# Kernel tuning notes

Hardware: AMD Instinct MI355X
Metric: run time of the kernel (lower is better)

The kernel has to match this reference:

```python
import jax, jax.numpy as jnp
import numpy as np

N, E = 50000, 600000
IN_DIM, H, D = 256, 4, 128
NEG_SLOPE = 0.2


def setup_inputs() -> dict:
    key = jax.random.key(0)
    ks = jax.random.split(key, 9)
    x = jax.random.normal(ks[0], (N, IN_DIM), dtype=jnp.float32)
    src = jax.random.randint(ks[1], (E,), 0, N, dtype=jnp.int32)
    dst = jax.random.randint(ks[2], (E,), 0, N, dtype=jnp.int32)
    # layer 0: in=256 -> H*D=512; layer 1: in=H*D=512 -> H*D=512
    s0 = 1.0 / np.sqrt(IN_DIM)
    s1 = 1.0 / np.sqrt(H * D)
    W0 = jax.random.normal(ks[3], (IN_DIM, H * D), dtype=jnp.float32) * s0
    al0 = jax.random.normal(ks[4], (H, D), dtype=jnp.float32) * s1
    ar0 = jax.random.normal(ks[5], (H, D), dtype=jnp.float32) * s1
    W1 = jax.random.normal(ks[6], (H * D, H * D), dtype=jnp.float32) * s1
    al1 = jax.random.normal(ks[7], (H, D), dtype=jnp.float32) * s1
    ar1 = jax.random.normal(ks[8], (H, D), dtype=jnp.float32) * s1
    return {"x": x, "src": src, "dst": dst,
            "W0": W0, "al0": al0, "ar0": ar0,
            "W1": W1, "al1": al1, "ar1": ar1}


def gat_conv(x, W, al, ar, src, dst):
    """One DGL-style GATConv layer. x:[N,in] -> out:[N,H,D] (post relu)."""
    h = (x @ W).reshape(N, H, D)                       # fc, no bias
    el = jnp.sum(h * al, axis=-1)                      # [N,H]
    er = jnp.sum(h * ar, axis=-1)                      # [N,H]
    e = jax.nn.leaky_relu(el[src] + er[dst], NEG_SLOPE)  # [E,H]
    # edge softmax over incoming edges of each dst node (numerically stable)
    m = jax.ops.segment_max(e, dst, num_segments=N)    # [N,H]
    m = jnp.where(jnp.isfinite(m), m, 0.0)             # empty segments -> -inf
    ex = jnp.exp(e - m[dst])                           # [E,H]
    denom = jax.ops.segment_sum(ex, dst, num_segments=N)  # [N,H]
    alpha = ex / denom[dst]                            # [E,H]
    msg = alpha[:, :, None] * h[src]                   # [E,H,D]
    rst = jax.ops.segment_sum(msg, dst, num_segments=N)  # [N,H,D]
    return jax.nn.relu(rst)                            # activation=F.relu


def reference(x, src, dst, W0, al0, ar0, W1, al1, ar1):
    h = gat_conv(x, W0, al0, ar0, src, dst)            # [N,H,D]
    h = h.reshape(N, H * D)                            # flatten(1)
    h = gat_conv(h, W1, al1, ar1, src, dst)            # [N,H,D]
    return h.mean(axis=1)                              # mean over heads -> [N,D]
```

## Files before the change

kernel.cpp:

```cpp
#include <hip/hip_runtime.h>

#define NN 50000
#define NE 600000
#define DD 128
#define HD 512
#define NB 196

typedef unsigned short u16;
typedef __attribute__((ext_vector_type(8))) short short8;
typedef __attribute__((ext_vector_type(4))) float floatx4;

__device__ inline float b2f(u16 u) {
  return __uint_as_float(((unsigned int)u) << 16);
}
__device__ inline u16 f2b(float f) {
  unsigned int u = __float_as_uint(f);
  u = u + 0x7FFFu + ((u >> 16) & 1u);
  return (u16)(u >> 16);
}

__device__ inline void load_lds16(const u16* g, u16* l) {
  __builtin_amdgcn_global_load_lds(
      (const __attribute__((address_space(1))) unsigned int*)(uintptr_t)g,
      (__attribute__((address_space(3))) unsigned int*)(uintptr_t)l,
      16, 0, 0);
}

__global__ void zero_k(int* __restrict__ p, int n) {
  int i = blockIdx.x * 256 + threadIdx.x;
  if (i < n) p[i] = 0;
}

__global__ void transpose_k(const float* __restrict__ W, u16* __restrict__ Wt, int K) {
  int idx = blockIdx.x * 256 + threadIdx.x;
  if (idx >= K * 512) return;
  int k = idx >> 9, n = idx & 511;
  Wt[n * K + k] = f2b(W[idx]);
}

__global__ void count_k(const int* __restrict__ dst, int* __restrict__ counts) {
  int e = blockIdx.x * 256 + threadIdx.x;
  if (e < NE) atomicAdd(&counts[dst[e]], 1);
}

__global__ __launch_bounds__(256) void blockscan_k(const int* __restrict__ counts,
                                                   int* __restrict__ rowp,
                                                   int* __restrict__ bsums) {
  __shared__ int tmp[256];
  int t = threadIdx.x;
  int i = blockIdx.x * 256 + t;
  int v = (i < NN) ? counts[i] : 0;
  tmp[t] = v;
  __syncthreads();
  for (int off = 1; off < 256; off <<= 1) {
    int u = (t >= off) ? tmp[t - off] : 0;
    __syncthreads();
    tmp[t] += u;
    __syncthreads();
  }
  if (i < NN) rowp[i] = tmp[t] - v;
  if (t == 255) bsums[blockIdx.x] = tmp[t];
}

__global__ __launch_bounds__(256) void bscan_k(const int* __restrict__ bsums,
                                               int* __restrict__ boffs) {
  __shared__ int tmp[256];
  int t = threadIdx.x;
  int v = (t < NB) ? bsums[t] : 0;
  tmp[t] = v;
  __syncthreads();
  for (int off = 1; off < 256; off <<= 1) {
    int u = (t >= off) ? tmp[t - off] : 0;
    __syncthreads();
    tmp[t] += u;
    __syncthreads();
  }
  if (t < NB) boffs[t] = tmp[t] - v;
}

__global__ void addoff_k(int* __restrict__ rowp, int* __restrict__ cursor,
                         const int* __restrict__ boffs) {
  int i = blockIdx.x * 256 + threadIdx.x;
  if (i < NN) {
    int v = rowp[i] + boffs[blockIdx.x];
    rowp[i] = v;
    cursor[i] = v;
  }
  if (i == 0) rowp[NN] = NE;
}

__global__ void scatter_k(const int* __restrict__ src, const int* __restrict__ dst,
                          int* __restrict__ cursor, int* __restrict__ csrs) {
  int e = blockIdx.x * 256 + threadIdx.x;
  if (e < NE) {
    int d = dst[e];
    int pos = atomicAdd(&cursor[d], 1);
    csrs[pos] = src[e];
  }
}

template <int K, bool A_F32>
__global__ __launch_bounds__(512) void gemm_el_er(
    const void* __restrict__ Ap, const u16* __restrict__ Wt,
    const float* __restrict__ al, const float* __restrict__ ar,
    u16* __restrict__ h, float* __restrict__ el, float* __restrict__ er) {
  __shared__ u16 Wt_s[2][512 * 32];

  const int tid = threadIdx.x;
  const int w = tid >> 6, lane = tid & 63, quad = lane >> 4, l16 = lane & 15;
  const int rg = w >> 1, cg = w & 1;
  const int bm = blockIdx.x;

  floatx4 acc[16] = {};

  const int rowA = bm * 64 + rg * 16 + l16;
  const long arow = (rowA < NN) ? rowA : (NN - 1);

  const int drow = lane >> 2;
  const int q8 = ((lane & 3) ^ ((lane >> 3) & 3)) * 8;
  const int p4 = (quad ^ ((l16 >> 1) & 3)) * 8;

  const float* Af = (const float*)Ap;
  const u16* Ab = (const u16*)Ap;

#define ISSUE_DMA(kk, sel)                                                  \
  {                                                                         \
    _Pragma("unroll") for (int rr = 0; rr < 4; ++rr) {                      \
      const int rbase = rr * 128 + w * 16;                                  \
      load_lds16(Wt + (long)(rbase + drow) * K + (kk) + q8,                 \
                 &Wt_s[sel][rbase * 32]);                                   \
    }                                                                       \
  }

  floatx4 a0A, a1A, a0B, a1B;
  short8 rawA, rawB;

#define ISSUE_A(kk, a0r, a1r, rawr)                                         \
  {                                                                         \
    if (A_F32) {                                                            \
      a0r = *(const floatx4*)(Af + arow * K + (kk) + quad * 8);             \
      a1r = *(const floatx4*)(Af + arow * K + (kk) + quad * 8 + 4);         \
    } else {                                                                \
      rawr = *(const short8*)(Ab + arow * K + (kk) + quad * 8);             \
    }                                                                       \
  }

#define CVT_A(af, a0r, a1r, rawr)                                           \
  short8 af;                                                                \
  {                                                                         \
    if (A_F32) {                                                            \
      u16 tmp[8];                                                           \
      _Pragma("unroll") for (int j = 0; j < 4; ++j) tmp[j] = f2b(a0r[j]);   \
      _Pragma("unroll") for (int j = 0; j < 4; ++j) tmp[4 + j] = f2b(a1r[j]); \
      af = *(short8*)tmp;                                                   \
    } else {                                                                \
      af = rawr;                                                            \
    }                                                                       \
  }

#define WAIT_PREV()                                                         \
  {                                                                         \
    if (A_F32)                                                              \
      asm volatile("s_waitcnt vmcnt(6)" ::: "memory");                      \
    else                                                                    \
      asm volatile("s_waitcnt vmcnt(5)" ::: "memory");                      \
  }

  const int T = K / 32;

  ISSUE_A(0, a0A, a1A, rawA);
  ISSUE_DMA(0, 0);

  for (int t = 0; t < T; t += 2) {
    {
      const int k1 = (t + 1) * 32;
      ISSUE_A(k1, a0B, a1B, rawB);
      ISSUE_DMA(k1, 1);
      WAIT_PREV();
      __builtin_amdgcn_s_barrier();
      CVT_A(af, a0A, a1A, rawA);
#pragma unroll
      for (int ct = 0; ct < 16; ++ct) {
        short8 bf = *(const short8*)(&Wt_s[0][(cg * 256 + ct * 16 + l16) * 32 + p4]);
        acc[ct] = __builtin_amdgcn_mfma_f32_16x16x32_bf16(af, bf, acc[ct], 0, 0, 0);
      }
      __builtin_amdgcn_sched_barrier(0);
      __builtin_amdgcn_s_barrier();
    }
    {
      const int t2 = (t + 2 < T) ? t + 2 : T - 1;
      const int k2 = t2 * 32;
      ISSUE_A(k2, a0A, a1A, rawA);
      ISSUE_DMA(k2, 0);
      WAIT_PREV();
      __builtin_amdgcn_s_barrier();
      CVT_A(af, a0B, a1B, rawB);
#pragma unroll
      for (int ct = 0; ct < 16; ++ct) {
        short8 bf = *(const short8*)(&Wt_s[1][(cg * 256 + ct * 16 + l16) * 32 + p4]);
        acc[ct] = __builtin_amdgcn_mfma_f32_16x16x32_bf16(af, bf, acc[ct], 0, 0, 0);
      }
      __builtin_amdgcn_sched_barrier(0);
      __builtin_amdgcn_s_barrier();
    }
  }

#undef ISSUE_DMA
#undef ISSUE_A
#undef CVT_A
#undef WAIT_PREV

  float alv[16], arv[16];
#pragma unroll
  for (int ct = 0; ct < 16; ++ct) {
    int col = cg * 256 + ct * 16 + l16;
    alv[ct] = al[col];
    arv[ct] = ar[col];
  }
#pragma unroll
  for (int reg = 0; reg < 4; ++reg) {
    const int r = bm * 64 + rg * 16 + quad * 4 + reg;
    float pel[2] = {0.f, 0.f}, per_[2] = {0.f, 0.f};
#pragma unroll
    for (int ct = 0; ct < 16; ++ct) {
      int hh = ct >> 3;
      float v = acc[ct][reg];
      pel[hh] += v * alv[ct];
      per_[hh] += v * arv[ct];
    }
#pragma unroll
    for (int m = 1; m < 16; m <<= 1) {
      pel[0] += __shfl_xor(pel[0], m, 64);
      pel[1] += __shfl_xor(pel[1], m, 64);
      per_[0] += __shfl_xor(per_[0], m, 64);
      per_[1] += __shfl_xor(per_[1], m, 64);
    }
    if (r < NN) {
#pragma unroll
      for (int ct = 0; ct < 16; ++ct)
        h[(long)r * HD + cg * 256 + ct * 16 + l16] = f2b(acc[ct][reg]);
      if (l16 == 0) {
        el[r * 4 + cg * 2] = pel[0];
        el[r * 4 + cg * 2 + 1] = pel[1];
        er[r * 4 + cg * 2] = per_[0];
        er[r * 4 + cg * 2 + 1] = per_[1];
      }
    }
  }
}

template <int MODE>
__global__ __launch_bounds__(256) void aggregate(
    const u16* __restrict__ h, const float* __restrict__ el,
    const float* __restrict__ er, const int* __restrict__ rowp,
    const int* __restrict__ csrs, u16* __restrict__ ob, float* __restrict__ of) {
  __shared__ float w_s[4][64][4];
  const int wv = threadIdx.x >> 6, lane = threadIdx.x & 63;
  const int n = blockIdx.x * 4 + wv;
  if (n >= NN) return;
  const int base = rowp[n];
  const int deg = rowp[n + 1] - base;
  const int head = lane >> 4;

  if (deg == 0) {
    if (MODE == 0) {
      short8 z = {};
      *(short8*)(ob + (long)n * HD + lane * 8) = z;
    } else if (lane < 16) {
      floatx4 z = {};
      __builtin_nontemporal_store(z, (floatx4*)(of + (long)n * DD + lane * 8));
      __builtin_nontemporal_store(z, (floatx4*)(of + (long)n * DD + lane * 8 + 4));
    }
    return;
  }

  const floatx4 er4 = *(const floatx4*)(er + n * 4);

  float acc[8] = {0.f, 0.f, 0.f, 0.f, 0.f, 0.f, 0.f, 0.f};
  float sm0 = 0.f, sm1 = 0.f, sm2 = 0.f, sm3 = 0.f;

  for (int c0 = 0; c0 < deg; c0 += 64) {
    const int cnt = min(deg - c0, 64);

    const int l = c0 + lane;
    const int idx = csrs[base + ((l < deg) ? l : (deg - 1))];
    const floatx4 el4 = *(const floatx4*)(el + (long)idx * 4);
    floatx4 w4;
#pragma unroll
    for (int j = 0; j < 4; ++j) {
      float e = el4[j] + er4[j];
      e = (e > 0.f) ? e : 0.2f * e;
      w4[j] = (l < deg) ? __expf(e) : 0.f;
    }
    sm0 += w4[0];
    sm1 += w4[1];
    sm2 += w4[2];
    sm3 += w4[3];
    *(floatx4*)(&w_s[wv][lane][0]) = w4;

    for (int i = 0; i < cnt; i += 8) {
      short8 hv[8];
#pragma unroll
      for (int u = 0; u < 8; ++u) {
        const int s = __builtin_amdgcn_readlane(idx, i + u);
        hv[u] = *(const short8*)(h + (long)s * HD + lane * 8);
      }
#pragma unroll
      for (int u = 0; u < 8; ++u) {
        const float w = w_s[wv][i + u][head];
#pragma unroll
        for (int j = 0; j < 8; ++j) acc[j] += w * b2f((u16)hv[u][j]);
      }
    }
  }

#pragma unroll
  for (int m = 1; m < 64; m <<= 1) {
    sm0 += __shfl_xor(sm0, m, 64);
    sm1 += __shfl_xor(sm1, m, 64);
    sm2 += __shfl_xor(sm2, m, 64);
    sm3 += __shfl_xor(sm3, m, 64);
  }
  const float sm = (head == 0) ? sm0 : (head == 1) ? sm1 : (head == 2) ? sm2 : sm3;

  const float inv = 1.f / sm;
#pragma unroll
  for (int j = 0; j < 8; ++j) acc[j] = fmaxf(acc[j] * inv, 0.f);

  if (MODE == 0) {
    u16 ub[8];
#pragma unroll
    for (int j = 0; j < 8; ++j) ub[j] = f2b(acc[j]);
    *(short8*)(ob + (long)n * HD + lane * 8) = *(short8*)ub;
  } else {
#pragma unroll
    for (int j = 0; j < 8; ++j) acc[j] += __shfl_xor(acc[j], 16, 64);
#pragma unroll
    for (int j = 0; j < 8; ++j) acc[j] += __shfl_xor(acc[j], 32, 64);
    if (lane < 16) {
      floatx4 o0, o1;
#pragma unroll
      for (int j = 0; j < 4; ++j) o0[j] = acc[j] * 0.25f;
#pragma unroll
      for (int j = 0; j < 4; ++j) o1[j] = acc[4 + j] * 0.25f;
      __builtin_nontemporal_store(o0, (floatx4*)(of + (long)n * DD + lane * 8));
      __builtin_nontemporal_store(o1, (floatx4*)(of + (long)n * DD + lane * 8 + 4));
    }
  }
}

extern "C" void kernel_launch(void* const* d_in, const int* in_sizes, int n_in,
                              void* d_out, int out_size, void* d_ws, size_t ws_size,
                              hipStream_t stream) {
  const float* x = (const float*)d_in[0];
  const int* src = (const int*)d_in[1];
  const int* dst = (const int*)d_in[2];
  const float* W0 = (const float*)d_in[3];
  const float* al0 = (const float*)d_in[4];
  const float* ar0 = (const float*)d_in[5];
  const float* W1 = (const float*)d_in[6];
  const float* al1 = (const float*)d_in[7];
  const float* ar1 = (const float*)d_in[8];
  float* out = (float*)d_out;

  char* p = (char*)d_ws;
  u16* h = (u16*)p;        p += (size_t)NN * HD * 2;
  u16* rst0 = (u16*)p;     p += (size_t)NN * HD * 2;
  float* el = (float*)p;   p += (size_t)NN * 4 * 4;
  float* er = (float*)p;   p += (size_t)NN * 4 * 4;
  u16* Wt0 = (u16*)p;      p += 512 * 256 * 2;
  u16* Wt1 = (u16*)p;      p += 512 * 512 * 2;
  int* counts = (int*)p;   p += (size_t)NN * 4;
  int* cursor = (int*)p;   p += (size_t)NN * 4;
  int* rowp = (int*)p;     p += (size_t)(NN + 1) * 4;
  int* bsums = (int*)p;    p += 256 * 4;
  int* boffs = (int*)p;    p += 256 * 4;
  int* csrs = (int*)p;     p += (size_t)NE * 4;

  zero_k<<<NB, 256, 0, stream>>>(counts, NN);
  count_k<<<(NE + 255) / 256, 256, 0, stream>>>(dst, counts);
  blockscan_k<<<NB, 256, 0, stream>>>(counts, rowp, bsums);
  bscan_k<<<1, 256, 0, stream>>>(bsums, boffs);
  addoff_k<<<NB, 256, 0, stream>>>(rowp, cursor, boffs);
  scatter_k<<<(NE + 255) / 256, 256, 0, stream>>>(src, dst, cursor, csrs);
  transpose_k<<<(256 * 512 + 255) / 256, 256, 0, stream>>>(W0, Wt0, 256);
  transpose_k<<<(512 * 512 + 255) / 256, 256, 0, stream>>>(W1, Wt1, 512);

  const int gblocks = (NN + 63) / 64;
  gemm_el_er<256, true><<<gblocks, 512, 0, stream>>>(x, Wt0, al0, ar0, h, el, er);
  aggregate<0><<<(NN + 3) / 4, 256, 0, stream>>>(h, el, er, rowp, csrs, rst0, nullptr);
  gemm_el_er<512, false><<<gblocks, 512, 0, stream>>>(rst0, Wt1, al1, ar1, h, el, er);
  aggregate<1><<<(NN + 3) / 4, 256, 0, stream>>>(h, el, er, rowp, csrs, nullptr, out);
}
```

Measured before the change: 466.3 us.

## Split layer-0 aggregation across 8 column chunks per node

Replaces the layer-0 aggregate kernel with a variant that launches 8 blocks per group of nodes, each handling a 64-column chunk (one half-head). Within a wave, 8 edge groups of 8 lanes gather short8 slices of neighbor features, and the partial sums are then reduced with shuffles. The aim is more parallelism and better gather concurrency for low-degree nodes. In exchange, each block recomputes the edge weights and reloads the CSR indices, the softmax uses no max subtraction, and the grid is eight times larger.

After: 526.8 us. 1.13x slower.

```diff
diff --git a/kernel.cpp b/kernel.cpp
--- a/kernel.cpp
+++ b/kernel.cpp
@@ -249,6 +249,77 @@
   }
 }
 
+__global__ __launch_bounds__(256) void aggregate_c8(
+    const u16* __restrict__ h, const float* __restrict__ el,
+    const float* __restrict__ er, const int* __restrict__ rowp,
+    const int* __restrict__ csrs, u16* __restrict__ ob) {
+  __shared__ float w_s[4][64];
+  __shared__ int is_s[4][64];
+  const int b = blockIdx.x;
+  const int chunk = b & 7;
+  const int wv = threadIdx.x >> 6, lane = threadIdx.x & 63;
+  const int n = (b >> 3) * 4 + wv;
+  const int hc = chunk >> 1;
+  const int eg = lane >> 3, cl = lane & 7;
+  const long coff = chunk * 64 + cl * 8;
+
+  const int base = rowp[n];
+  const int deg = rowp[n + 1] - base;
+
+  if (deg == 0) {
+    if (eg == 0) {
+      short8 z = {};
+      *(short8*)(ob + (long)n * HD + coff) = z;
+    }
+    return;
+  }
+
+  const float er_h = er[n * 4 + hc];
+  float acc[8] = {0.f, 0.f, 0.f, 0.f, 0.f, 0.f, 0.f, 0.f};
+  float smp = 0.f;
+
+  for (int c0 = 0; c0 < deg; c0 += 64) {
+    const int l = c0 + lane;
+    const int idx = csrs[base + ((l < deg) ? l : (deg - 1))];
+    float e = el[idx * 4 + hc] + er_h;
+    e = (e > 0.f) ? e : 0.2f * e;
+    const float w = (l < deg) ? __expf(e) : 0.f;
+    smp += w;
+    w_s[wv][lane] = w;
+    is_s[wv][lane] = idx;
+    const int cnt = (deg - c0 < 64) ? (deg - c0) : 64;
+    for (int i = 0; i < cnt; i += 16) {
+      const int s0 = is_s[wv][i + eg];
+      const int s1 = is_s[wv][i + 8 + eg];
+      const float wa = w_s[wv][i + eg];
+      const float wb = w_s[wv][i + 8 + eg];
+      const short8 hv0 = *(const short8*)(h + (long)s0 * HD + coff);
+      const short8 hv1 = *(const short8*)(h + (long)s1 * HD + coff);
+#pragma unroll
+      for (int j = 0; j < 8; ++j) acc[j] += wa * b2f((u16)hv0[j]);
+#pragma unroll
+      for (int j = 0; j < 8; ++j) acc[j] += wb * b2f((u16)hv1[j]);
+    }
+  }
+
+#pragma unroll
+  for (int j = 0; j < 8; ++j) {
+    acc[j] += __shfl_xor(acc[j], 8, 64);
+    acc[j] += __shfl_xor(acc[j], 16, 64);
+    acc[j] += __shfl_xor(acc[j], 32, 64);
+  }
+#pragma unroll
+  for (int m = 1; m < 64; m <<= 1) smp += __shfl_xor(smp, m, 64);
+  const float inv = 1.f / smp;
+
+  if (eg == 0) {
+    u16 ub[8];
+#pragma unroll
+    for (int j = 0; j < 8; ++j) ub[j] = f2b(fmaxf(acc[j] * inv, 0.f));
+    *(short8*)(ob + (long)n * HD + coff) = *(short8*)ub;
+  }
+}
+
 template <int MODE>
 __global__ __launch_bounds__(256) void aggregate(
     const u16* __restrict__ h, const float* __restrict__ el,
@@ -388,7 +459,7 @@
 
   const int gblocks = (NN + 63) / 64;
   gemm_el_er<256, true><<<gblocks, 512, 0, stream>>>(x, Wt0, al0, ar0, h, el, er);
-  aggregate<0><<<(NN + 3) / 4, 256, 0, stream>>>(h, el, er, rowp, csrs, rst0, nullptr);
+  aggregate_c8<<<12500 * 8, 256, 0, stream>>>(h, el, er, rowp, csrs, rst0);
   gemm_el_er<512, false><<<gblocks, 512, 0, stream>>>(rst0, Wt1, al1, ar1, h, el, er);
   aggregate<1><<<(NN + 3) / 4, 256, 0, stream>>>(h, el, er, rowp, csrs, nullptr, out);
 }
```

## Split GEMM column halves across blocks and merge small setup kernels

Applied to the files above, without the earlier changes.

The GEMM now launches twice as many 256-thread blocks, each computing a 64x256 output tile, instead of 512-thread blocks covering all 512 columns. This halves the LDS buffer per block to raise occupancy. The K loop becomes fully unrolled with a wait-all plus barrier per step, replacing the partial-vmcnt two-stage pipeline. Separately, the two weight transposes are fused into one launch and the block-offset scan is folded into addoff_k, cutting launch count. The split makes each A tile be loaded twice and weakens load/compute overlap.

Result: no change. 473.3 us (+1.5%).

```diff
diff --git a/kernel.cpp b/kernel.cpp
--- a/kernel.cpp
+++ b/kernel.cpp
@@ -31,11 +31,19 @@
   if (i < n) p[i] = 0;
 }
 
-__global__ void transpose_k(const float* __restrict__ W, u16* __restrict__ Wt, int K) {
+__global__ void transpose2_k(const float* __restrict__ W0, u16* __restrict__ Wt0,
+                             const float* __restrict__ W1, u16* __restrict__ Wt1) {
   int idx = blockIdx.x * 256 + threadIdx.x;
-  if (idx >= K * 512) return;
-  int k = idx >> 9, n = idx & 511;
-  Wt[n * K + k] = f2b(W[idx]);
+  if (idx < 256 * 512) {
+    int k = idx >> 9, n = idx & 511;
+    Wt0[n * 256 + k] = f2b(W0[idx]);
+  } else {
+    idx -= 256 * 512;
+    if (idx < 512 * 512) {
+      int k = idx >> 9, n = idx & 511;
+      Wt1[n * 512 + k] = f2b(W1[idx]);
+    }
+  }
 }
 
 __global__ void count_k(const int* __restrict__ dst, int* __restrict__ counts) {
@@ -62,8 +70,9 @@
   if (t == 255) bsums[blockIdx.x] = tmp[t];
 }
 
-__global__ __launch_bounds__(256) void bscan_k(const int* __restrict__ bsums,
-                                               int* __restrict__ boffs) {
+__global__ __launch_bounds__(256) void addoff_k(int* __restrict__ rowp,
+                                                int* __restrict__ cursor,
+                                                const int* __restrict__ bsums) {
   __shared__ int tmp[256];
   int t = threadIdx.x;
   int v = (t < NB) ? bsums[t] : 0;
@@ -75,16 +84,12 @@
     tmp[t] += u;
     __syncthreads();
   }
-  if (t < NB) boffs[t] = tmp[t] - v;
-}
-
-__global__ void addoff_k(int* __restrict__ rowp, int* __restrict__ cursor,
-                         const int* __restrict__ boffs) {
-  int i = blockIdx.x * 256 + threadIdx.x;
+  const int boff = (blockIdx.x == 0) ? 0 : tmp[blockIdx.x - 1];
+  int i = blockIdx.x * 256 + t;
   if (i < NN) {
-    int v = rowp[i] + boffs[blockIdx.x];
-    rowp[i] = v;
-    cursor[i] = v;
+    int v2 = rowp[i] + boff;
+    rowp[i] = v2;
+    cursor[i] = v2;
   }
   if (i == 0) rowp[NN] = NE;
 }
@@ -100,20 +105,21 @@
 }
 
 template <int K, bool A_F32>
-__global__ __launch_bounds__(512) void gemm_el_er(
+__global__ __launch_bounds__(256) void gemm_el_er(
     const void* __restrict__ Ap, const u16* __restrict__ Wt,
     const float* __restrict__ al, const float* __restrict__ ar,
     u16* __restrict__ h, float* __restrict__ el, float* __restrict__ er) {
-  __shared__ u16 Wt_s[2][512 * 32];
+  __shared__ u16 Wt_s[2][256 * 32];
 
   const int tid = threadIdx.x;
   const int w = tid >> 6, lane = tid & 63, quad = lane >> 4, l16 = lane & 15;
-  const int rg = w >> 1, cg = w & 1;
-  const int bm = blockIdx.x;
+  const int b = blockIdx.x;
+  const int bm = b >> 1, bn = b & 1;
+  const int colbase = bn << 8;
 
   floatx4 acc[16] = {};
 
-  const int rowA = bm * 64 + rg * 16 + l16;
+  const int rowA = bm * 64 + w * 16 + l16;
   const long arow = (rowA < NN) ? rowA : (NN - 1);
 
   const int drow = lane >> 2;
@@ -126,8 +132,8 @@
 #define ISSUE_DMA(kk, sel)                                                  \
   {                                                                         \
     _Pragma("unroll") for (int rr = 0; rr < 4; ++rr) {                      \
-      const int rbase = rr * 128 + w * 16;                                  \
-      load_lds16(Wt + (long)(rbase + drow) * K + (kk) + q8,                 \
+      const int rbase = w * 64 + rr * 16;                                   \
+      load_lds16(Wt + (long)(colbase + rbase + drow) * K + (kk) + q8,       \
                  &Wt_s[sel][rbase * 32]);                                   \
     }                                                                       \
   }
@@ -145,81 +151,72 @@
     }                                                                       \
   }
 
-#define CVT_A(af, a0r, a1r, rawr)                                           \
-  short8 af;                                                                \
+#define MFMA16(sel, af)                                                     \
   {                                                                         \
+    _Pragma("unroll") for (int ct = 0; ct < 16; ++ct) {                     \
+      short8 bf =                                                           \
+          *(const short8*)(&Wt_s[sel][(ct * 16 + l16) * 32 + p4]);          \
+      acc[ct] =                                                             \
+          __builtin_amdgcn_mfma_f32_16x16x32_bf16(af, bf, acc[ct], 0, 0, 0);\
+    }                                                                       \
+  }
+
+#define CVT_MFMA(sel, a0r, a1r, rawr)                                       \
+  {                                                                         \
+    short8 af;                                                              \
     if (A_F32) {                                                            \
       u16 tmp[8];                                                           \
       _Pragma("unroll") for (int j = 0; j < 4; ++j) tmp[j] = f2b(a0r[j]);   \
-      _Pragma("unroll") for (int j = 0; j < 4; ++j) tmp[4 + j] = f2b(a1r[j]); \
+      _Pragma("unroll") for (int j = 0; j < 4; ++j) tmp[4 + j] =            \
+          f2b(a1r[j]);                                                      \
       af = *(short8*)tmp;                                                   \
     } else {                                                                \
       af = rawr;                                                            \
     }                                                                       \
-  }
-
-#define WAIT_PREV()                                                         \
-  {                                                                         \
-    if (A_F32)                                                              \
-      asm volatile("s_waitcnt vmcnt(6)" ::: "memory");                      \
-    else                                                                    \
-      asm volatile("s_waitcnt vmcnt(5)" ::: "memory");                      \
+    MFMA16(sel, af);                                                        \
   }
 
   const int T = K / 32;
 
   ISSUE_A(0, a0A, a1A, rawA);
   ISSUE_DMA(0, 0);
-
-  for (int t = 0; t < T; t += 2) {
-    {
-      const int k1 = (t + 1) * 32;
-      ISSUE_A(k1, a0B, a1B, rawB);
-      ISSUE_DMA(k1, 1);
-      WAIT_PREV();
-      __builtin_amdgcn_s_barrier();
-      CVT_A(af, a0A, a1A, rawA);
-#pragma unroll
-      for (int ct = 0; ct < 16; ++ct) {
-        short8 bf = *(const short8*)(&Wt_s[0][(cg * 256 + ct * 16 + l16) * 32 + p4]);
-        acc[ct] = __builtin_amdgcn_mfma_f32_16x16x32_bf16(af, bf, acc[ct], 0, 0, 0);
+  asm volatile("s_waitcnt vmcnt(0)" ::: "memory");
+  __builtin_amdgcn_s_barrier();
+
+#pragma unroll
+  for (int t = 0; t < T; ++t) {
+    if (t + 1 < T) {
+      if ((t & 1) == 0) {
+        ISSUE_A((t + 1) * 32, a0B, a1B, rawB);
+      } else {
+        ISSUE_A((t + 1) * 32, a0A, a1A, rawA);
       }
-      __builtin_amdgcn_sched_barrier(0);
-      __builtin_amdgcn_s_barrier();
-    }
-    {
-      const int t2 = (t + 2 < T) ? t + 2 : T - 1;
-      const int k2 = t2 * 32;
-      ISSUE_A(k2, a0A, a1A, rawA);
-      ISSUE_DMA(k2, 0);
-      WAIT_PREV();
-      __builtin_amdgcn_s_barrier();
-      CVT_A(af, a0B, a1B, rawB);
-#pragma unroll
-      for (int ct = 0; ct < 16; ++ct) {
-        short8 bf = *(const short8*)(&Wt_s[1][(cg * 256 + ct * 16 + l16) * 32 + p4]);
-        acc[ct] = __builtin_amdgcn_mfma_f32_16x16x32_bf16(af, bf, acc[ct], 0, 0, 0);
-      }
-      __builtin_amdgcn_sched_barrier(0);
-      __builtin_amdgcn_s_barrier();
-    }
+      ISSUE_DMA((t + 1) * 32, (t + 1) & 1);
+    }
+    if ((t & 1) == 0) {
+      CVT_MFMA(0, a0A, a1A, rawA);
+    } else {
+      CVT_MFMA(1, a0B, a1B, rawB);
+    }
+    asm volatile("s_waitcnt vmcnt(0)" ::: "memory");
+    __builtin_amdgcn_s_barrier();
   }
 
 #undef ISSUE_DMA
 #undef ISSUE_A
-#undef CVT_A
-#undef WAIT_PREV
+#undef MFMA16
+#undef CVT_MFMA
 
   float alv[16], arv[16];
 #pragma unroll
   for (int ct = 0; ct < 16; ++ct) {
-    int col = cg * 256 + ct * 16 + l16;
+    int col = colbase + ct * 16 + l16;
     alv[ct] = al[col];
     arv[ct] = ar[col];
   }
 #pragma unroll
   for (int reg = 0; reg < 4; ++reg) {
-    const int r = bm * 64 + rg * 16 + quad * 4 + reg;
+    const int r = bm * 64 + w * 16 + quad * 4 + reg;
     float pel[2] = {0.f, 0.f}, per_[2] = {0.f, 0.f};
 #pragma unroll
     for (int ct = 0; ct < 16; ++ct) {
@@ -238,12 +235,12 @@
     if (r < NN) {
 #pragma unroll
       for (int ct = 0; ct < 16; ++ct)
-        h[(long)r * HD + cg * 256 + ct * 16 + l16] = f2b(acc[ct][reg]);
+        h[(long)r * HD + colbase + ct * 16 + l16] = f2b(acc[ct][reg]);
       if (l16 == 0) {
-        el[r * 4 + cg * 2] = pel[0];
-        el[r * 4 + cg * 2 + 1] = pel[1];
-        er[r * 4 + cg * 2] = per_[0];
-        er[r * 4 + cg * 2 + 1] = per_[1];
+        el[r * 4 + bn * 2] = pel[0];
+        el[r * 4 + bn * 2 + 1] = pel[1];
+        er[r * 4 + bn * 2] = per_[0];
+        er[r * 4 + bn * 2 + 1] = per_[1];
       }
     }
   }
@@ -374,21 +371,19 @@
   int* cursor = (int*)p;   p += (size_t)NN * 4;
   int* rowp = (int*)p;     p += (size_t)(NN + 1) * 4;
   int* bsums = (int*)p;    p += 256 * 4;
-  int* boffs = (int*)p;    p += 256 * 4;
   int* csrs = (int*)p;     p += (size_t)NE * 4;
 
   zero_k<<<NB, 256, 0, stream>>>(counts, NN);
   count_k<<<(NE + 255) / 256, 256, 0, stream>>>(dst, counts);
   blockscan_k<<<NB, 256, 0, stream>>>(counts, rowp, bsums);
-  bscan_k<<<1, 256, 0, stream>>>(bsums, boffs);
-  addoff_k<<<NB, 256, 0, stream>>>(rowp, cursor, boffs);
+  addoff_k<<<NB, 256, 0, stream>>>(rowp, cursor, bsums);
   scatter_k<<<(NE + 255) / 256, 256, 0, stream>>>(src, dst, cursor, csrs);
-  transpose_k<<<(256 * 512 + 255) / 256, 256, 0, stream>>>(W0, Wt0, 256);
-  transpose_k<<<(512 * 512 + 255) / 256, 256, 0, stream>>>(W1, Wt1, 512);
-
-  const int gblocks = (NN + 63) / 64;
-  gemm_el_er<256, true><<<gblocks, 512, 0, stream>>>(x, Wt0, al0, ar0, h, el, er);
+  transpose2_k<<<(256 * 512 + 512 * 512 + 255) / 256, 256, 0, stream>>>(
+      W0, Wt0, W1, Wt1);
+
+  const int gblocks = 2 * ((NN + 63) / 64);
+  gemm_el_er<256, true><<<gblocks, 256, 0, stream>>>(x, Wt0, al0, ar0, h, el, er);
   aggregate<0><<<(NN + 3) / 4, 256, 0, stream>>>(h, el, er, rowp, csrs, rst0, nullptr);
-  gemm_el_er<512, false><<<gblocks, 512, 0, stream>>>(rst0, Wt1, al1, ar1, h, el, er);
+  gemm_el_er<512, false><<<gblocks, 256, 0, stream>>>(rst0, Wt1, al1, ar1, h, el, er);
   aggregate<1><<<(NN + 3) / 4, 256, 0, stream>>>(h, el, er, rowp, csrs, nullptr, out);
 }
```
